# Performance work log

Hardware: AMD Instinct MI355X
Metric: run time of the kernel (lower is better)

The kernel has to match this reference:

```python
import jax, jax.numpy as jnp
import numpy as np

NG, ND, D, H = 50000, 20000, 128, 128
EGG, EGDA, ELAB = 800000, 400000, 200000
EPS, SLOPE = 1e-5, 0.01


def setup_inputs() -> dict:
    key = jax.random.key(0)
    ks = jax.random.split(key, 24)
    w = lambda k, s: jax.random.normal(k, s, jnp.float32) * 0.05
    return {
        "x_gene": jax.random.normal(ks[0], (NG, D), jnp.float32),
        "x_disease": jax.random.normal(ks[1], (ND, D), jnp.float32),
        "W_dst1": w(ks[2], (3, D, H)), "W_src1": w(ks[3], (3, D, H)),
        "W_upd1": w(ks[4], (3, 2 * H, H)),
        "b_dst1": w(ks[5], (3, H)), "b_src1": w(ks[6], (3, H)), "b_upd1": w(ks[7], (3, H)),
        "W_dst2": w(ks[8], (3, H, H)), "W_src2": w(ks[9], (3, H, H)),
        "W_upd2": w(ks[10], (3, 2 * H, H)),
        "b_dst2": w(ks[11], (3, H)), "b_src2": w(ks[12], (3, H)), "b_upd2": w(ks[13], (3, H)),
        "bn_gamma": jnp.ones((2, H), jnp.float32), "bn_beta": jnp.zeros((2, H), jnp.float32),
        "gg_src": jax.random.randint(ks[14], (EGG,), 0, NG, jnp.int32),
        "gg_dst": jax.random.randint(ks[15], (EGG,), 0, NG, jnp.int32),
        "gda_src": jax.random.randint(ks[16], (EGDA,), 0, NG, jnp.int32),
        "gda_dst": jax.random.randint(ks[17], (EGDA,), 0, ND, jnp.int32),
        "label_src": jax.random.randint(ks[18], (ELAB,), 0, NG, jnp.int32),
        "label_dst": jax.random.randint(ks[19], (ELAB,), 0, ND, jnp.int32),
    }


def _mean_agg(x_src, src_idx, dst_idx, n_dst):
    # matmul(adj_t, x_src, reduce='mean'): per-dst mean of neighbor features (0 if no in-edges)
    s = jax.ops.segment_sum(x_src[src_idx], dst_idx, num_segments=n_dst)
    deg = jax.ops.segment_sum(jnp.ones((src_idx.shape[0],), x_src.dtype), dst_idx, num_segments=n_dst)
    return s / jnp.maximum(deg, 1.0)[:, None]


def _conv(i, x_src, x_dst, src_idx, dst_idx, n_dst, Wd, Ws, Wu, bd, bs, bu):
    agg = _mean_agg(x_src, src_idx, dst_idx, n_dst)
    dst_msg = x_dst @ Wd[i] + bd[i]
    src_msg = agg @ Ws[i] + bs[i]
    return jnp.concatenate([dst_msg, src_msg], axis=1) @ Wu[i] + bu[i]


def _layer(xg, xd, Wd, Ws, Wu, bd, bs, bu, gg_src, gg_dst, gda_src, gda_dst):
    out_gg = _conv(0, xg, xg, gg_src, gg_dst, NG, Wd, Ws, Wu, bd, bs, bu)    # gene -> gene
    out_gda = _conv(1, xg, xd, gda_src, gda_dst, ND, Wd, Ws, Wu, bd, bs, bu)  # gene -> disease
    out_rev = _conv(2, xd, xg, gda_dst, gda_src, NG, Wd, Ws, Wu, bd, bs, bu)  # disease -> gene (reverse edges)
    gene = 0.5 * (out_gg + out_rev)  # stack+mean across edge types for gene dst
    return gene, out_gda


def _bn(x, g, b):
    # BatchNorm1d in training mode: batch stats over node dim, biased variance
    m = jnp.mean(x, axis=0)
    v = jnp.mean((x - m) ** 2, axis=0)
    return (x - m) * jax.lax.rsqrt(v + EPS) * g + b


def _lrelu(x):
    return jnp.where(x >= 0, x, SLOPE * x)


def reference(x_gene, x_disease, W_dst1, W_src1, W_upd1, b_dst1, b_src1, b_upd1,
              W_dst2, W_src2, W_upd2, b_dst2, b_src2, b_upd2, bn_gamma, bn_beta,
              gg_src, gg_dst, gda_src, gda_dst, label_src, label_dst):
    g, d = _layer(x_gene, x_disease, W_dst1, W_src1, W_upd1, b_dst1, b_src1, b_upd1,
                  gg_src, gg_dst, gda_src, gda_dst)
    g = _lrelu(_bn(g, bn_gamma[0], bn_beta[0]))
    d = _lrelu(_bn(d, bn_gamma[1], bn_beta[1]))
    g, d = _layer(g, d, W_dst2, W_src2, W_upd2, b_dst2, b_src2, b_upd2,
                  gg_src, gg_dst, gda_src, gda_dst)
    # dot-product decoder on supervision (gene, gda, disease) label edges
    return jnp.sum(g[label_src] * d[label_dst], axis=-1)
```

## Files before the change

### kernel.cpp

```cpp
#include <hip/hip_runtime.h>
#include <hip/hip_bf16.h>
#include <cstddef>

#define NG   50000
#define ND   20000
#define DH   128
#define EGG  800000
#define EGDA 400000
#define ELAB 200000

#define B1G 391
#define B1D 157
#define TB  939
#define TBP 940
#define PB0 0
#define PB1 (NG+1)
#define PB2 (NG+1+ND+1)

typedef __hip_bfloat16  bf16;
typedef __attribute__((ext_vector_type(8))) short bf16x8;
typedef __attribute__((ext_vector_type(4))) float f32x4;

__device__ __forceinline__ float bf2f(short s){
  return __uint_as_float(((unsigned)(unsigned short)s) << 16);
}
__device__ __forceinline__ unsigned short f2b(float x){
  unsigned u = __float_as_uint(x);
  return (unsigned short)((u + 0x7FFF + ((u >> 16) & 1)) >> 16);
}

__global__ __launch_bounds__(256) void k_hist1(const int* __restrict__ k0, const int* __restrict__ k1,
                                               const int* __restrict__ k2, int* __restrict__ hist){
  __shared__ int lh[400];
  const int g = blockIdx.y;
  const int n  = (g == 0) ? EGG : EGDA;
  const int B1 = (g == 1) ? B1D : B1G;
  const int bb = (g == 0) ? 0 : (g == 1 ? B1G : B1G + B1D);
  const int* key = (g == 0) ? k0 : (g == 1 ? k1 : k2);
  for (int t = threadIdx.x; t < B1; t += 256) lh[t] = 0;
  __syncthreads();
  for (int i = blockIdx.x*blockDim.x + threadIdx.x; i < n; i += gridDim.x*blockDim.x)
    atomicAdd(&lh[key[i] >> 7], 1);
  __syncthreads();
  for (int t = threadIdx.x; t < B1; t += 256){
    int c = lh[t];
    if (c) atomicAdd(&hist[bb + t], c);
  }
}

__global__ __launch_bounds__(1024) void k_exscan(const int* __restrict__ cnt,
                                                 int* __restrict__ ptr, int* __restrict__ cur, int n){
  __shared__ int wsum[16];
  __shared__ int carry;
  const int tid = threadIdx.x, lane = tid & 63, wid = tid >> 6;
  if (tid == 0) carry = 0;
  __syncthreads();
  for (int base = 0; base < n; base += 4096){
    int i0 = base + tid*4;
    int4 v = {0,0,0,0};
    if (i0 < n) v = *(const int4*)(cnt + i0);
    int tsum = v.x + v.y + v.z + v.w;
    int x = tsum;
    #pragma unroll
    for (int off = 1; off < 64; off <<= 1){
      int t = __shfl_up(x, off);
      if (lane >= off) x += t;
    }
    if (lane == 63) wsum[wid] = x;
    __syncthreads();
    if (wid == 0 && lane < 16){
      int w = wsum[lane];
      #pragma unroll
      for (int off = 1; off < 16; off <<= 1){
        int t = __shfl_up(w, off);
        if (lane >= off) w += t;
      }
      wsum[lane] = w;
    }
    __syncthreads();
    int waveoff = wid ? wsum[wid-1] : 0;
    if (i0 < n){
      int ex = carry + waveoff + x - tsum;
      int4 o;
      o.x = ex; o.y = ex + v.x; o.z = o.y + v.y; o.w = o.z + v.z;
      *(int4*)(ptr + i0) = o;
      *(int4*)(cur + i0) = o;
    }
    int total = wsum[15];
    __syncthreads();
    if (tid == 0) carry += total;
    __syncthreads();
  }
  if (tid == 0) ptr[n] = carry;
}

__global__ __launch_bounds__(256) void k_scatter1(const int* __restrict__ k0, const int* __restrict__ v0,
                                                  const int* __restrict__ k1, const int* __restrict__ v1,
                                                  int* __restrict__ gcur, unsigned* __restrict__ pk){
  __shared__ int lh[400];
  __shared__ int base[400];
  const int g = blockIdx.y;
  const int n  = (g == 0) ? EGG : EGDA;
  const int B1 = (g == 1) ? B1D : B1G;
  const int bb = (g == 0) ? 0 : (g == 1 ? B1G : B1G + B1D);
  const int* key = (g == 0) ? k0 : (g == 1 ? k1 : v1);
  const int* val = (g == 0) ? v0 : (g == 1 ? v1 : k1);
  const int tid = threadIdx.x;
  const int chunk0 = blockIdx.x*4096;
  if (chunk0 >= n) return;
  for (int t = tid; t < B1; t += 256) lh[t] = 0;
  __syncthreads();
  int kd[16], vv[16];
  #pragma unroll
  for (int it = 0; it < 16; ++it){
    int i = chunk0 + it*256 + tid;
    int k = -1, v = 0;
    if (i < n){ k = key[i]; v = val[i]; atomicAdd(&lh[k >> 7], 1); }
    kd[it] = k; vv[it] = v;
  }
  __syncthreads();
  for (int t = tid; t < B1; t += 256){
    int c = lh[t];
    base[t] = c ? atomicAdd(&gcur[bb + t], c) : 0;
    lh[t] = 0;
  }
  __syncthreads();
  #pragma unroll
  for (int it = 0; it < 16; ++it){
    int k = kd[it];
    if (k >= 0){
      int b = k >> 7;
      int p = base[b] + atomicAdd(&lh[b], 1);
      pk[p] = ((unsigned)(k & 127) << 17) | (unsigned)vv[it];
    }
  }
}

__global__ __launch_bounds__(256) void k_csr2(const unsigned* __restrict__ pk,
                                              const int* __restrict__ gbase,
                                              int* __restrict__ ptr_all, int* __restrict__ col){
  __shared__ int lh[128];
  __shared__ int cur[128];
  __shared__ int sh0;
  const int b = blockIdx.x, tid = threadIdx.x;
  int lb, pbase, Ngr, bend;
  if (b < B1G)            { lb = b;             pbase = PB0; Ngr = NG; bend = B1G; }
  else if (b < B1G + B1D) { lb = b - B1G;       pbase = PB1; Ngr = ND; bend = B1G + B1D; }
  else                    { lb = b - B1G - B1D; pbase = PB2; Ngr = NG; bend = TB; }
  const int s = gbase[b], e = gbase[b+1];
  if (tid < 128) lh[tid] = 0;
  __syncthreads();
  for (int i = s + tid; i < e; i += 256)
    atomicAdd(&lh[(pk[i] >> 17) & 127], 1);
  __syncthreads();
  int lane = tid & 63;
  int v = 0, x = 0;
  if (tid < 128){
    v = lh[tid]; x = v;
    #pragma unroll
    for (int o = 1; o < 64; o <<= 1){
      int t = __shfl_up(x, o);
      if (lane >= o) x += t;
    }
    if (tid == 63) sh0 = x;
  }
  __syncthreads();
  if (tid < 128){
    int excl = x - v + (tid >= 64 ? sh0 : 0);
    cur[tid] = s + excl;
    int loc = (lb << 7) + tid;
    if (loc < Ngr) ptr_all[pbase + loc] = s + excl;
  }
  __syncthreads();
  for (int i = s + tid; i < e; i += 256){
    unsigned p = pk[i];
    int dl = (p >> 17) & 127;
    int pos = atomicAdd(&cur[dl], 1);
    col[pos] = (int)(p & 0x1FFFFu);
  }
  if (lb == 0 && tid == 0) ptr_all[pbase + Ngr] = gbase[bend];
}

#define PREP_F2B_BLOCKS (((NG+ND)*32)/256)
__global__ __launch_bounds__(256) void k_prep(
    const float* __restrict__ Wd1, const float* __restrict__ Ws1, const float* __restrict__ Wu1,
    const float* __restrict__ Wd2, const float* __restrict__ Ws2, const float* __restrict__ Wu2,
    const float* __restrict__ bd1, const float* __restrict__ bs1, const float* __restrict__ bu1,
    const float* __restrict__ bd2, const float* __restrict__ bs2, const float* __restrict__ bu2,
    float* __restrict__ AB, float* __restrict__ cv,
    const float* __restrict__ Xg, const float* __restrict__ Xd,
    unsigned short* __restrict__ Yg, unsigned short* __restrict__ Yd){
  const int b = blockIdx.x, tid = threadIdx.x;
  if (b < 768){
    int idx = b*256 + tid;
    int layer = idx / 98304;
    int r0 = idx - layer*98304;
    int mat = r0 >> 14;
    int r   = (r0 >> 7) & 127;
    int c   = r0 & 127;
    int i   = mat >> 1;
    int isB = mat & 1;
    const float* Wd = layer ? Wd2 : Wd1;
    const float* Ws = layer ? Ws2 : Ws1;
    const float* Wu = layer ? Wu2 : Wu1;
    const float* P = (isB ? Ws : Wd) + i*16384 + r*128;
    const float* Q = Wu + i*32768 + (isB ? 16384 : 0) + c;
    float s = 0.f;
    for (int h = 0; h < 128; ++h) s += P[h] * Q[h*128];
    AB[idx] = s;
  } else if (b < 771){
    int idx = (b - 768)*256 + tid;
    if (idx >= 768) return;
    int layer = idx / 384;
    int r = idx - layer*384;
    int i = r >> 7, h = r & 127;
    const float* bd = layer ? bd2 : bd1;
    const float* bs = layer ? bs2 : bs1;
    const float* bu = layer ? bu2 : bu1;
    const float* Wu = layer ? Wu2 : Wu1;
    float s = bu[i*128 + h];
    const float* Ut = Wu + i*32768 + h;
    const float* Ub = Ut + 16384;
    for (int k = 0; k < 128; ++k)
      s += bd[i*128 + k] * Ut[k*128] + bs[i*128 + k] * Ub[k*128];
    cv[idx] = s;
  } else {
    int idx = (b - 771)*256 + tid;
    const int GQ = NG*32;
    const float* X; unsigned short* Y; int i;
    if (idx < GQ){ X = Xg; Y = Yg; i = idx; }
    else         { X = Xd; Y = Yd; i = idx - GQ; }
    float4 v = ((const float4*)X)[i];
    ushort4 o;
    o.x = f2b(v.x); o.y = f2b(v.y); o.z = f2b(v.z); o.w = f2b(v.w);
    ((ushort4*)Y)[i] = o;
  }
}

__global__ __launch_bounds__(256) void k_pack(const float* __restrict__ AB, const float* __restrict__ cv,
                                              bf16* __restrict__ Wg1, bf16* __restrict__ Wd1p,
                                              bf16* __restrict__ Wg2, bf16* __restrict__ Wd2p,
                                              float* __restrict__ cg1, float* __restrict__ cd1,
                                              float* __restrict__ cg2, float* __restrict__ cd2){
  int idx = blockIdx.x*256 + threadIdx.x;
  int layer = idx / 81920;
  int rem = idx - layer*81920;
  const float* ABl = AB + layer*98304;
  const float* cvl = cv + layer*384;
  if (rem < 49152){
    int n0  = rem / 6144;
    int r2  = rem - n0*6144;
    int ks  = r2 >> 9;
    int lane = (r2 >> 3) & 63;
    int j   = r2 & 7;
    int k   = ks*32 + (lane >> 4)*8 + j;
    int c   = n0*16 + (lane & 15);
    float v;
    if      (k < 128) v = 0.5f*(ABl[0*16384 + k*128 + c] + ABl[4*16384 + k*128 + c]);
    else if (k < 256) v = 0.5f* ABl[1*16384 + (k-128)*128 + c];
    else              v = 0.5f* ABl[5*16384 + (k-256)*128 + c];
    bf16* W = layer ? Wg2 : Wg1;
    ((unsigned short*)W)[rem] = f2b(v);
    if (rem < 128){
      float* cg = layer ? cg2 : cg1;
      cg[rem] = 0.5f*(cvl[rem] + cvl[256 + rem]);
    }
  } else {
    int d = rem - 49152;
    int n0  = d >> 12;
    int ks  = (d >> 9) & 7;
    int lane = (d >> 3) & 63;
    int j   = d & 7;
    int k   = ks*32 + (lane >> 4)*8 + j;
    int c   = n0*16 + (lane & 15);
    float v = (k < 128) ? ABl[2*16384 + k*128 + c] : ABl[3*16384 + (k-128)*128 + c];
    bf16* W = layer ? Wd2p : Wd1p;
    ((unsigned short*)W)[d] = f2b(v);
    if (d < 128){
      float* cd = layer ? cd2 : cd1;
      cd[d] = cvl[128 + d];
    }
  }
}

__global__ __launch_bounds__(256) void k_agg(const bf16* __restrict__ Xg, const bf16* __restrict__ Xd,
    const int* __restrict__ ptr_all, const int* __restrict__ col,
    bf16* __restrict__ OutGG, bf16* __restrict__ OutGDA, bf16* __restrict__ OutREV){
  int q = (blockIdx.x*256 + threadIdx.x) >> 4;
  int lane = threadIdx.x & 15;
  const bf16* X; bf16* Out; const int* ptr; int dst;
  if (q < NG)          { X = Xg; Out = OutGG;  ptr = ptr_all + PB0; dst = q; }
  else if (q < NG+ND)  { X = Xg; Out = OutGDA; ptr = ptr_all + PB1; dst = q - NG; }
  else                 { X = Xd; Out = OutREV; ptr = ptr_all + PB2; dst = q - NG - ND; }
  int s = ptr[dst], e = ptr[dst+1];
  float a[8];
  #pragma unroll
  for (int j = 0; j < 8; ++j) a[j] = 0.f;
  const size_t loff = (size_t)lane*8;
  int i = s;
  for (; i + 8 <= e; i += 8){
    bf16x8 v0 = *(const bf16x8*)(X + (size_t)col[i  ]*DH + loff);
    bf16x8 v1 = *(const bf16x8*)(X + (size_t)col[i+1]*DH + loff);
    bf16x8 v2 = *(const bf16x8*)(X + (size_t)col[i+2]*DH + loff);
    bf16x8 v3 = *(const bf16x8*)(X + (size_t)col[i+3]*DH + loff);
    bf16x8 v4 = *(const bf16x8*)(X + (size_t)col[i+4]*DH + loff);
    bf16x8 v5 = *(const bf16x8*)(X + (size_t)col[i+5]*DH + loff);
    bf16x8 v6 = *(const bf16x8*)(X + (size_t)col[i+6]*DH + loff);
    bf16x8 v7 = *(const bf16x8*)(X + (size_t)col[i+7]*DH + loff);
    #pragma unroll
    for (int j = 0; j < 8; ++j)
      a[j] += ((bf2f(v0[j]) + bf2f(v1[j])) + (bf2f(v2[j]) + bf2f(v3[j])))
            + ((bf2f(v4[j]) + bf2f(v5[j])) + (bf2f(v6[j]) + bf2f(v7[j])));
  }
  for (; i + 4 <= e; i += 4){
    bf16x8 v0 = *(const bf16x8*)(X + (size_t)col[i  ]*DH + loff);
    bf16x8 v1 = *(const bf16x8*)(X + (size_t)col[i+1]*DH + loff);
    bf16x8 v2 = *(const bf16x8*)(X + (size_t)col[i+2]*DH + loff);
    bf16x8 v3 = *(const bf16x8*)(X + (size_t)col[i+3]*DH + loff);
    #pragma unroll
    for (int j = 0; j < 8; ++j)
      a[j] += (bf2f(v0[j]) + bf2f(v1[j])) + (bf2f(v2[j]) + bf2f(v3[j]));
  }
  for (; i < e; ++i){
    bf16x8 v = *(const bf16x8*)(X + (size_t)col[i]*DH + loff);
    #pragma unroll
    for (int j = 0; j < 8; ++j) a[j] += bf2f(v[j]);
  }
  float inv = 1.f / fmaxf((float)(e - s), 1.f);
  bf16x8 o;
  #pragma unroll
  for (int j = 0; j < 8; ++j) o[j] = (short)f2b(a[j]*inv);
  *(bf16x8*)(Out + (size_t)dst*DH + loff) = o;
}

template<int KS>
__device__ __forceinline__ void gemm_body(
    const bf16* __restrict__ X0, const bf16* __restrict__ X1, const bf16* __restrict__ X2,
    const bf16* __restrict__ Wp, const float* __restrict__ cvec,
    unsigned short* __restrict__ Out, int M, int blk){
  const int tid = threadIdx.x;
  const int wave = tid >> 6, lane = tid & 63;
  const int lrow = lane & 15, quad = lane >> 4;
  const int row0 = blk*64;
  const bf16* Xs[3] = {X0, X1, X2};
  f32x4 acc[2][4];
  #pragma unroll
  for (int p = 0; p < 2; ++p)
    #pragma unroll
    for (int t = 0; t < 4; ++t) acc[p][t] = 0.0f;
  const bf16x8* wp = (const bf16x8*)Wp;
  const int f00 = (2*wave*KS)*64 + lane;
  #pragma unroll
  for (int ks = 0; ks < KS; ++ks){
    const bf16* Xm = Xs[ks >> 2];
    const int kk = (ks & 3)*32 + quad*8;
    bf16x8 a[4];
    #pragma unroll
    for (int t = 0; t < 4; ++t){
      int ar = row0 + t*16 + lrow; if (ar > M-1) ar = M-1;
      a[t] = *(const bf16x8*)(Xm + (size_t)ar*DH + kk);
    }
    bf16x8 b0 = wp[f00 + ks*64];
    bf16x8 b1 = wp[f00 + (KS + ks)*64];
    #pragma unroll
    for (int t = 0; t < 4; ++t){
      acc[0][t] = __builtin_amdgcn_mfma_f32_16x16x32_bf16(a[t], b0, acc[0][t], 0, 0, 0);
      acc[1][t] = __builtin_amdgcn_mfma_f32_16x16x32_bf16(a[t], b1, acc[1][t], 0, 0, 0);
    }
  }
  #pragma unroll
  for (int p = 0; p < 2; ++p){
    int c = (2*wave + p)*16 + lrow;
    float cb = cvec[c];
    #pragma unroll
    for (int t = 0; t < 4; ++t){
      #pragma unroll
      for (int r = 0; r < 4; ++r){
        int row = row0 + t*16 + quad*4 + r;
        if (row < M) Out[(size_t)row*DH + c] = f2b(acc[p][t][r] + cb);
      }
    }
  }
}

#define GBGENE ((NG+63)/64)
#define GBDIS  ((ND+63)/64)

__global__ __launch_bounds__(256) void k_gemm(
    const bf16* __restrict__ Xg, const bf16* __restrict__ Ag, const bf16* __restrict__ Rg,
    const bf16* __restrict__ Wg, const float* __restrict__ cg, unsigned short* __restrict__ Og,
    const bf16* __restrict__ Xd, const bf16* __restrict__ Ad,
    const bf16* __restrict__ Wd, const float* __restrict__ cd, unsigned short* __restrict__ Od){
  if ((int)blockIdx.x < GBGENE)
    gemm_body<12>(Xg, Ag, Rg, Wg, cg, Og, NG, blockIdx.x);
  else
    gemm_body<8>(Xd, Ad, Ad, Wd, cd, Od, ND, blockIdx.x - GBGENE);
}

#define SBG 192
#define SBD 64
__global__ __launch_bounds__(256) void k_bn_stats(const bf16* __restrict__ Xgb, const bf16* __restrict__ Xdb,
                                                  float* __restrict__ sums){
  __shared__ float acc[256];
  int tid = threadIdx.x;
  acc[tid] = 0.f;
  __syncthreads();
  int g = (int)blockIdx.x >= SBG;
  int bidx = blockIdx.x - (g ? SBG : 0);
  int NB = g ? SBD : SBG;
  int N  = g ? ND : NG;
  const bf16* Xb = g ? Xdb : Xgb;
  float* sm = sums + g*256;
  int c8 = (tid & 15)*8;
  int rl = tid >> 4;
  float s[8], q[8];
  #pragma unroll
  for (int j = 0; j < 8; ++j){ s[j] = 0.f; q[j] = 0.f; }
  for (int r = bidx*16 + rl; r < N; r += NB*16){
    bf16x8 v = *(const bf16x8*)(Xb + (size_t)r*DH + c8);
    #pragma unroll
    for (int j = 0; j < 8; ++j){
      float f = bf2f(v[j]);
      s[j] += f; q[j] += f*f;
    }
  }
  #pragma unroll
  for (int j = 0; j < 8; ++j){
    atomicAdd(&acc[c8+j], s[j]);
    atomicAdd(&acc[128+c8+j], q[j]);
  }
  __syncthreads();
  atomicAdd(&sm[tid], acc[tid]);
}

__global__ __launch_bounds__(256) void k_bn_apply(const bf16* __restrict__ Xgb, const bf16* __restrict__ Xdb,
    const float* __restrict__ sums, const float* __restrict__ gamma, const float* __restrict__ beta,
    unsigned short* __restrict__ Yg, unsigned short* __restrict__ Yd){
  __shared__ float sc[256], sb[256];
  int tid = threadIdx.x;
  {
    int g = tid >> 7, c = tid & 127;
    float invN = g ? (1.f/ND) : (1.f/NG);
    const float* sm = sums + g*256;
    float m = sm[c]*invN;
    float v = sm[128 + c]*invN - m*m;
    float s = rsqrtf(v + 1e-5f) * gamma[g*128 + c];
    sc[tid] = s;
    sb[tid] = beta[g*128 + c] - m*s;
  }
  __syncthreads();
  const int GT = NG*16;
  const int TOT = GT + ND*16;
  for (int idx = blockIdx.x*256 + tid; idx < TOT; idx += gridDim.x*256){
    const bf16x8* src; bf16x8* dst; int i, cb;
    if (idx < GT){ src = (const bf16x8*)Xgb; dst = (bf16x8*)Yg; i = idx; cb = 0; }
    else         { src = (const bf16x8*)Xdb; dst = (bf16x8*)Yd; i = idx - GT; cb = 128; }
    bf16x8 v = src[i];
    int c = cb + (i & 15)*8;
    bf16x8 o;
    #pragma unroll
    for (int j = 0; j < 8; ++j){
      float y = bf2f(v[j])*sc[c+j] + sb[c+j];
      y = y >= 0.f ? y : 0.01f*y;
      o[j] = (short)f2b(y);
    }
    dst[i] = o;
  }
}

__global__ __launch_bounds__(256) void k_decode(const bf16* __restrict__ G, const bf16* __restrict__ Dd,
    const int* __restrict__ ls, const int* __restrict__ ld, float* __restrict__ out, int E){
  int p = (blockIdx.x*256 + threadIdx.x) >> 4;
  int lane = threadIdx.x & 15;
  int e0 = p*2, e1 = p*2 + 1;
  if (e0 >= E) return;
  int a0 = ls[e0], b0 = ld[e0];
  int a1 = ls[e1], b1 = ld[e1];
  const size_t loff = (size_t)lane*8;
  bf16x8 g0 = *(const bf16x8*)(G  + (size_t)a0*DH + loff);
  bf16x8 d0 = *(const bf16x8*)(Dd + (size_t)b0*DH + loff);
  bf16x8 g1 = *(const bf16x8*)(G  + (size_t)a1*DH + loff);
  bf16x8 d1 = *(const bf16x8*)(Dd + (size_t)b1*DH + loff);
  float s0 = 0.f, s1 = 0.f;
  #pragma unroll
  for (int j = 0; j < 8; ++j){
    s0 += bf2f(g0[j])*bf2f(d0[j]);
    s1 += bf2f(g1[j])*bf2f(d1[j]);
  }
  #pragma unroll
  for (int off = 8; off; off >>= 1){
    s0 += __shfl_down(s0, off, 16);
    s1 += __shfl_down(s1, off, 16);
  }
  if (lane == 0){ out[e0] = s0; out[e1] = s1; }
}

extern "C" void kernel_launch(void* const* d_in, const int* in_sizes, int n_in,
                              void* d_out, int out_size, void* d_ws, size_t ws_size,
                              hipStream_t stream){
  const float* x_gene = (const float*)d_in[0];
  const float* x_dis  = (const float*)d_in[1];
  const float* Wd1 = (const float*)d_in[2];
  const float* Ws1 = (const float*)d_in[3];
  const float* Wu1 = (const float*)d_in[4];
  const float* bd1 = (const float*)d_in[5];
  const float* bs1 = (const float*)d_in[6];
  const float* bu1 = (const float*)d_in[7];
  const float* Wd2 = (const float*)d_in[8];
  const float* Ws2 = (const float*)d_in[9];
  const float* Wu2 = (const float*)d_in[10];
  const float* bd2 = (const float*)d_in[11];
  const float* bs2 = (const float*)d_in[12];
  const float* bu2 = (const float*)d_in[13];
  const float* bng = (const float*)d_in[14];
  const float* bnb = (const float*)d_in[15];
  const int* gg_src  = (const int*)d_in[16];
  const int* gg_dst  = (const int*)d_in[17];
  const int* gda_src = (const int*)d_in[18];
  const int* gda_dst = (const int*)d_in[19];
  const int* lsrc = (const int*)d_in[20];
  const int* ldst = (const int*)d_in[21];

  char* ws = (char*)d_ws;
  size_t off = 0;
  auto alloc = [&](size_t bytes)->void*{
    void* p = ws + off; off += (bytes + 255) & ~(size_t)255; return p;
  };
  int* hist    = (int*)alloc(960*4);
  float* bnsum = (float*)alloc(2*256*4);
  int* gbase   = (int*)alloc(960*4);
  int* gcur    = (int*)alloc(960*4);
  int* ptr_all = (int*)alloc((size_t)(NG+1+ND+1+NG+1)*4);
  int* col     = (int*)alloc((size_t)(EGG+2*EGDA)*4);
  unsigned* pk = (unsigned*)alloc((size_t)(EGG+2*EGDA)*4);
  float* AB  = (float*)alloc(2*98304*4);
  float* cv  = (float*)alloc(2*384*4);
  float* cg1 = (float*)alloc(128*4);
  float* cd1 = (float*)alloc(128*4);
  float* cg2 = (float*)alloc(128*4);
  float* cd2 = (float*)alloc(128*4);
  bf16* Wg1  = (bf16*)alloc(49152*2);
  bf16* Wp1  = (bf16*)alloc(32768*2);
  bf16* Wg2  = (bf16*)alloc(49152*2);
  bf16* Wp2  = (bf16*)alloc(32768*2);
  bf16* xgb  = (bf16*)alloc((size_t)NG*DH*2);
  bf16* xdb  = (bf16*)alloc((size_t)ND*DH*2);
  bf16* aggGGb  = (bf16*)alloc((size_t)NG*DH*2);
  bf16* aggREVb = (bf16*)alloc((size_t)NG*DH*2);
  bf16* aggGDAb = (bf16*)alloc((size_t)ND*DH*2);
  bf16* Xg2b = (bf16*)alloc((size_t)NG*DH*2);
  bf16* Xd2b = (bf16*)alloc((size_t)ND*DH*2);
  bf16* outgb = (bf16*)alloc((size_t)NG*DH*2);
  bf16* outdb = (bf16*)alloc((size_t)ND*DH*2);

  hipMemsetAsync(hist, 0, 960*4 + 512*4, stream);

  {
    dim3 gh(96, 3);
    k_hist1<<<gh,256,0,stream>>>(gg_dst, gda_dst, gda_src, hist);
    k_exscan<<<1,1024,0,stream>>>(hist, gbase, gcur, TBP);
    dim3 gs(196, 3);
    k_scatter1<<<gs,256,0,stream>>>(gg_dst, gg_src, gda_dst, gda_src, gcur, pk);
    k_csr2<<<TB,256,0,stream>>>(pk, gbase, ptr_all, col);
  }

  k_prep<<<771 + PREP_F2B_BLOCKS,256,0,stream>>>(
      Wd1, Ws1, Wu1, Wd2, Ws2, Wu2, bd1, bs1, bu1, bd2, bs2, bu2,
      AB, cv, x_gene, x_dis, (unsigned short*)xgb, (unsigned short*)xdb);
  k_pack<<<640,256,0,stream>>>(AB, cv, Wg1, Wp1, Wg2, Wp2, cg1, cd1, cg2, cd2);

  k_agg<<<(NG+ND+NG)*16/256,256,0,stream>>>(xgb, xdb, ptr_all, col, aggGGb, aggGDAb, aggREVb);
  k_gemm<<<GBGENE+GBDIS,256,0,stream>>>(xgb, aggGGb, aggREVb, Wg1, cg1, (unsigned short*)outgb,
                                        xdb, aggGDAb, Wp1, cd1, (unsigned short*)outdb);
  k_bn_stats<<<SBG+SBD,256,0,stream>>>(outgb, outdb, bnsum);
  k_bn_apply<<<1024,256,0,stream>>>(outgb, outdb, bnsum, bng, bnb,
                                    (unsigned short*)Xg2b, (unsigned short*)Xd2b);

  k_agg<<<(NG+ND+NG)*16/256,256,0,stream>>>(Xg2b, Xd2b, ptr_all, col, aggGGb, aggGDAb, aggREVb);
  k_gemm<<<GBGENE+GBDIS,256,0,stream>>>(Xg2b, aggGGb, aggREVb, Wg2, cg2, (unsigned short*)outgb,
                                        Xd2b, aggGDAb, Wp2, cd2, (unsigned short*)outdb);

  k_decode<<<ELAB*16/2/256,256,0,stream>>>(outgb, outdb, lsrc, ldst, (float*)d_out, ELAB);
}
```

Before: 390.1 us.

## Gather neighbor features from FP8 copies in mean aggregation

```diff
diff --git a/kernel.cpp b/kernel.cpp
--- a/kernel.cpp
+++ b/kernel.cpp
@@ -20,6 +20,7 @@
 typedef __hip_bfloat16  bf16;
 typedef __attribute__((ext_vector_type(8))) short bf16x8;
 typedef __attribute__((ext_vector_type(4))) float f32x4;
+typedef __attribute__((ext_vector_type(2))) float f32x2;
 
 __device__ __forceinline__ float bf2f(short s){
   return __uint_as_float(((unsigned)(unsigned short)s) << 16);
@@ -27,6 +28,55 @@
 __device__ __forceinline__ unsigned short f2b(float x){
   unsigned u = __float_as_uint(x);
   return (unsigned short)((u + 0x7FFF + ((u >> 16) & 1)) >> 16);
+}
+
+__device__ __forceinline__ float fp8_dec1(unsigned v){
+  unsigned s = (v >> 7) & 1, e = (v >> 3) & 15, m = v & 7;
+  float r = e ? __uint_as_float(((e + 120) << 23) | (m << 20))
+              : (float)m * 0.001953125f;
+  return s ? -r : r;
+}
+__device__ __forceinline__ unsigned fp8_enc1(float x){
+  float a = fabsf(x);
+  if (a > 448.f) a = 448.f;
+  unsigned sgn = (__float_as_uint(x) >> 31) << 7;
+  unsigned res;
+  if (a < 0.015625f){
+    res = (unsigned)__float2int_rn(a * 512.f);
+    if (res > 7) res = 8;
+    if (res == 8) res = 0x08;
+  } else {
+    unsigned ab = __float_as_uint(a);
+    unsigned r = ab + 0x0007FFFF + ((ab >> 20) & 1);
+    int e = (int)(r >> 23) - 127;
+    unsigned m = (r >> 20) & 7;
+    if (e > 8){ e = 8; m = 6; }
+    res = ((unsigned)(e + 7) << 3) | m;
+  }
+  return res | sgn;
+}
+
+__device__ __forceinline__ void fp8x4_acc(unsigned w, float* a){
+#if __has_builtin(__builtin_amdgcn_cvt_pk_f32_fp8)
+  f32x2 p0 = __builtin_amdgcn_cvt_pk_f32_fp8((int)w, false);
+  f32x2 p1 = __builtin_amdgcn_cvt_pk_f32_fp8((int)w, true);
+  a[0] += p0.x; a[1] += p0.y; a[2] += p1.x; a[3] += p1.y;
+#else
+  a[0] += fp8_dec1(w & 255);
+  a[1] += fp8_dec1((w >> 8) & 255);
+  a[2] += fp8_dec1((w >> 16) & 255);
+  a[3] += fp8_dec1(w >> 24);
+#endif
+}
+__device__ __forceinline__ unsigned fp8x4_enc(float x0, float x1, float x2, float x3){
+#if __has_builtin(__builtin_amdgcn_cvt_pk_fp8_f32)
+  int v = 0;
+  v = __builtin_amdgcn_cvt_pk_fp8_f32(x0, x1, v, false);
+  v = __builtin_amdgcn_cvt_pk_fp8_f32(x2, x3, v, true);
+  return (unsigned)v;
+#else
+  return fp8_enc1(x0) | (fp8_enc1(x1) << 8) | (fp8_enc1(x2) << 16) | (fp8_enc1(x3) << 24);
+#endif
 }
 
 __global__ __launch_bounds__(256) void k_hist1(const int* __restrict__ k0, const int* __restrict__ k1,
@@ -189,7 +239,8 @@
     const float* __restrict__ bd2, const float* __restrict__ bs2, const float* __restrict__ bu2,
     float* __restrict__ AB, float* __restrict__ cv,
     const float* __restrict__ Xg, const float* __restrict__ Xd,
-    unsigned short* __restrict__ Yg, unsigned short* __restrict__ Yd){
+    unsigned short* __restrict__ Yg, unsigned short* __restrict__ Yd,
+    unsigned* __restrict__ Yg8, unsigned* __restrict__ Yd8){
   const int b = blockIdx.x, tid = threadIdx.x;
   if (b < 768){
     int idx = b*256 + tid;
@@ -227,13 +278,14 @@
   } else {
     int idx = (b - 771)*256 + tid;
     const int GQ = NG*32;
-    const float* X; unsigned short* Y; int i;
-    if (idx < GQ){ X = Xg; Y = Yg; i = idx; }
-    else         { X = Xd; Y = Yd; i = idx - GQ; }
+    const float* X; unsigned short* Y; unsigned* Y8; int i;
+    if (idx < GQ){ X = Xg; Y = Yg; Y8 = Yg8; i = idx; }
+    else         { X = Xd; Y = Yd; Y8 = Yd8; i = idx - GQ; }
     float4 v = ((const float4*)X)[i];
     ushort4 o;
     o.x = f2b(v.x); o.y = f2b(v.y); o.z = f2b(v.z); o.w = f2b(v.w);
     ((ushort4*)Y)[i] = o;
+    Y8[i] = fp8x4_enc(v.x, v.y, v.z, v.w);
   }
 }
 
@@ -283,54 +335,40 @@
   }
 }
 
-__global__ __launch_bounds__(256) void k_agg(const bf16* __restrict__ Xg, const bf16* __restrict__ Xd,
+__global__ __launch_bounds__(256) void k_agg(const unsigned* __restrict__ Xg8, const unsigned* __restrict__ Xd8,
     const int* __restrict__ ptr_all, const int* __restrict__ col,
     bf16* __restrict__ OutGG, bf16* __restrict__ OutGDA, bf16* __restrict__ OutREV){
   int q = (blockIdx.x*256 + threadIdx.x) >> 4;
   int lane = threadIdx.x & 15;
-  const bf16* X; bf16* Out; const int* ptr; int dst;
-  if (q < NG)          { X = Xg; Out = OutGG;  ptr = ptr_all + PB0; dst = q; }
-  else if (q < NG+ND)  { X = Xg; Out = OutGDA; ptr = ptr_all + PB1; dst = q - NG; }
-  else                 { X = Xd; Out = OutREV; ptr = ptr_all + PB2; dst = q - NG - ND; }
+  const unsigned* X; bf16* Out; const int* ptr; int dst;
+  if (q < NG)          { X = Xg8; Out = OutGG;  ptr = ptr_all + PB0; dst = q; }
+  else if (q < NG+ND)  { X = Xg8; Out = OutGDA; ptr = ptr_all + PB1; dst = q - NG; }
+  else                 { X = Xd8; Out = OutREV; ptr = ptr_all + PB2; dst = q - NG - ND; }
   int s = ptr[dst], e = ptr[dst+1];
   float a[8];
   #pragma unroll
   for (int j = 0; j < 8; ++j) a[j] = 0.f;
-  const size_t loff = (size_t)lane*8;
+  const int loff = lane*2;
   int i = s;
-  for (; i + 8 <= e; i += 8){
-    bf16x8 v0 = *(const bf16x8*)(X + (size_t)col[i  ]*DH + loff);
-    bf16x8 v1 = *(const bf16x8*)(X + (size_t)col[i+1]*DH + loff);
-    bf16x8 v2 = *(const bf16x8*)(X + (size_t)col[i+2]*DH + loff);
-    bf16x8 v3 = *(const bf16x8*)(X + (size_t)col[i+3]*DH + loff);
-    bf16x8 v4 = *(const bf16x8*)(X + (size_t)col[i+4]*DH + loff);
-    bf16x8 v5 = *(const bf16x8*)(X + (size_t)col[i+5]*DH + loff);
-    bf16x8 v6 = *(const bf16x8*)(X + (size_t)col[i+6]*DH + loff);
-    bf16x8 v7 = *(const bf16x8*)(X + (size_t)col[i+7]*DH + loff);
-    #pragma unroll
-    for (int j = 0; j < 8; ++j)
-      a[j] += ((bf2f(v0[j]) + bf2f(v1[j])) + (bf2f(v2[j]) + bf2f(v3[j])))
-            + ((bf2f(v4[j]) + bf2f(v5[j])) + (bf2f(v6[j]) + bf2f(v7[j])));
-  }
   for (; i + 4 <= e; i += 4){
-    bf16x8 v0 = *(const bf16x8*)(X + (size_t)col[i  ]*DH + loff);
-    bf16x8 v1 = *(const bf16x8*)(X + (size_t)col[i+1]*DH + loff);
-    bf16x8 v2 = *(const bf16x8*)(X + (size_t)col[i+2]*DH + loff);
-    bf16x8 v3 = *(const bf16x8*)(X + (size_t)col[i+3]*DH + loff);
-    #pragma unroll
-    for (int j = 0; j < 8; ++j)
-      a[j] += (bf2f(v0[j]) + bf2f(v1[j])) + (bf2f(v2[j]) + bf2f(v3[j]));
+    uint2 u0 = *(const uint2*)(X + (size_t)col[i  ]*32 + loff);
+    uint2 u1 = *(const uint2*)(X + (size_t)col[i+1]*32 + loff);
+    uint2 u2 = *(const uint2*)(X + (size_t)col[i+2]*32 + loff);
+    uint2 u3 = *(const uint2*)(X + (size_t)col[i+3]*32 + loff);
+    fp8x4_acc(u0.x, a);     fp8x4_acc(u0.y, a+4);
+    fp8x4_acc(u1.x, a);     fp8x4_acc(u1.y, a+4);
+    fp8x4_acc(u2.x, a);     fp8x4_acc(u2.y, a+4);
+    fp8x4_acc(u3.x, a);     fp8x4_acc(u3.y, a+4);
   }
   for (; i < e; ++i){
-    bf16x8 v = *(const bf16x8*)(X + (size_t)col[i]*DH + loff);
-    #pragma unroll
-    for (int j = 0; j < 8; ++j) a[j] += bf2f(v[j]);
+    uint2 u = *(const uint2*)(X + (size_t)col[i]*32 + loff);
+    fp8x4_acc(u.x, a);      fp8x4_acc(u.y, a+4);
   }
   float inv = 1.f / fmaxf((float)(e - s), 1.f);
   bf16x8 o;
   #pragma unroll
   for (int j = 0; j < 8; ++j) o[j] = (short)f2b(a[j]*inv);
-  *(bf16x8*)(Out + (size_t)dst*DH + loff) = o;
+  *(bf16x8*)(Out + (size_t)dst*DH + (size_t)lane*8) = o;
 }
 
 template<int KS>
@@ -435,7 +473,8 @@
 
 __global__ __launch_bounds__(256) void k_bn_apply(const bf16* __restrict__ Xgb, const bf16* __restrict__ Xdb,
     const float* __restrict__ sums, const float* __restrict__ gamma, const float* __restrict__ beta,
-    unsigned short* __restrict__ Yg, unsigned short* __restrict__ Yd){
+    unsigned short* __restrict__ Yg, unsigned short* __restrict__ Yd,
+    uint2* __restrict__ Yg8, uint2* __restrict__ Yd8){
   __shared__ float sc[256], sb[256];
   int tid = threadIdx.x;
   {
@@ -452,19 +491,25 @@
   const int GT = NG*16;
   const int TOT = GT + ND*16;
   for (int idx = blockIdx.x*256 + tid; idx < TOT; idx += gridDim.x*256){
-    const bf16x8* src; bf16x8* dst; int i, cb;
-    if (idx < GT){ src = (const bf16x8*)Xgb; dst = (bf16x8*)Yg; i = idx; cb = 0; }
-    else         { src = (const bf16x8*)Xdb; dst = (bf16x8*)Yd; i = idx - GT; cb = 128; }
+    const bf16x8* src; bf16x8* dst; uint2* dst8; int i, cb;
+    if (idx < GT){ src = (const bf16x8*)Xgb; dst = (bf16x8*)Yg; dst8 = Yg8; i = idx; cb = 0; }
+    else         { src = (const bf16x8*)Xdb; dst = (bf16x8*)Yd; dst8 = Yd8; i = idx - GT; cb = 128; }
     bf16x8 v = src[i];
     int c = cb + (i & 15)*8;
+    float y[8];
     bf16x8 o;
     #pragma unroll
     for (int j = 0; j < 8; ++j){
-      float y = bf2f(v[j])*sc[c+j] + sb[c+j];
-      y = y >= 0.f ? y : 0.01f*y;
-      o[j] = (short)f2b(y);
+      float t = bf2f(v[j])*sc[c+j] + sb[c+j];
+      t = t >= 0.f ? t : 0.01f*t;
+      y[j] = t;
+      o[j] = (short)f2b(t);
     }
     dst[i] = o;
+    uint2 p;
+    p.x = fp8x4_enc(y[0], y[1], y[2], y[3]);
+    p.y = fp8x4_enc(y[4], y[5], y[6], y[7]);
+    dst8[i] = p;
   }
 }
 
@@ -545,6 +590,10 @@
   bf16* Wp2  = (bf16*)alloc(32768*2);
   bf16* xgb  = (bf16*)alloc((size_t)NG*DH*2);
   bf16* xdb  = (bf16*)alloc((size_t)ND*DH*2);
+  unsigned* xg8  = (unsigned*)alloc((size_t)NG*DH);
+  unsigned* xd8  = (unsigned*)alloc((size_t)ND*DH);
+  unsigned* Xg28 = (unsigned*)alloc((size_t)NG*DH);
+  unsigned* Xd28 = (unsigned*)alloc((size_t)ND*DH);
   bf16* aggGGb  = (bf16*)alloc((size_t)NG*DH*2);
   bf16* aggREVb = (bf16*)alloc((size_t)NG*DH*2);
   bf16* aggGDAb = (bf16*)alloc((size_t)ND*DH*2);
@@ -566,17 +615,18 @@
 
   k_prep<<<771 + PREP_F2B_BLOCKS,256,0,stream>>>(
       Wd1, Ws1, Wu1, Wd2, Ws2, Wu2, bd1, bs1, bu1, bd2, bs2, bu2,
-      AB, cv, x_gene, x_dis, (unsigned short*)xgb, (unsigned short*)xdb);
+      AB, cv, x_gene, x_dis, (unsigned short*)xgb, (unsigned short*)xdb, xg8, xd8);
   k_pack<<<640,256,0,stream>>>(AB, cv, Wg1, Wp1, Wg2, Wp2, cg1, cd1, cg2, cd2);
 
-  k_agg<<<(NG+ND+NG)*16/256,256,0,stream>>>(xgb, xdb, ptr_all, col, aggGGb, aggGDAb, aggREVb);
+  k_agg<<<(NG+ND+NG)*16/256,256,0,stream>>>(xg8, xd8, ptr_all, col, aggGGb, aggGDAb, aggREVb);
   k_gemm<<<GBGENE+GBDIS,256,0,stream>>>(xgb, aggGGb, aggREVb, Wg1, cg1, (unsigned short*)outgb,
                                         xdb, aggGDAb, Wp1, cd1, (unsigned short*)outdb);
   k_bn_stats<<<SBG+SBD,256,0,stream>>>(outgb, outdb, bnsum);
   k_bn_apply<<<1024,256,0,stream>>>(outgb, outdb, bnsum, bng, bnb,
-                                    (unsigned short*)Xg2b, (unsigned short*)Xd2b);
-
-  k_agg<<<(NG+ND+NG)*16/256,256,0,stream>>>(Xg2b, Xd2b, ptr_all, col, aggGGb, aggGDAb, aggREVb);
+                                    (unsigned short*)Xg2b, (unsigned short*)Xd2b,
+                                    (uint2*)Xg28, (uint2*)Xd28);
+
+  k_agg<<<(NG+ND+NG)*16/256,256,0,stream>>>(Xg28, Xd28, ptr_all, col, aggGGb, aggGDAb, aggREVb);
   k_gemm<<<GBGENE+GBDIS,256,0,stream>>>(Xg2b, aggGGb, aggREVb, Wg2, cg2, (unsigned short*)outgb,
                                         Xd2b, aggGDAb, Wp2, cd2, (unsigned short*)outdb);
 
```

New measurement: 351.0 us. 1.11x faster.
